# Performance work log

Measured on AMD Instinct MI355X. Metric: run time of the kernel, lower is better.

## Reference

```python
import jax, jax.numpy as jnp
import numpy as np

D_K = 64

def setup_inputs() -> dict:
    key = jax.random.key(0)
    ks = jax.random.split(key, 5)
    B, H, N, Dk, Dv = 32, 16, 512, 64, 64
    Q = jax.random.normal(ks[0], (B, H, N, Dk), dtype=jnp.float32)
    K = jax.random.normal(ks[1], (B, H, N, Dk), dtype=jnp.float32)
    V = jax.random.normal(ks[2], (B, H, N, Dv), dtype=jnp.float32)
    pos_ids = jnp.arange(H * N, dtype=jnp.int64 if jax.config.jax_enable_x64 else jnp.int32).reshape(1, H, N)
    pos_k_table = jax.random.normal(ks[3], (H * N, Dk), dtype=jnp.float32)
    pos_v_table = jax.random.normal(ks[4], (H * N, Dv), dtype=jnp.float32)
    return {"Q": Q, "K": K, "V": V, "pos_ids": pos_ids,
            "pos_k_table": pos_k_table, "pos_v_table": pos_v_table}

def reference(Q, K, V, pos_ids, pos_k_table, pos_v_table):
    # Positional embedding lookup: [1, H, N, Dk] / [1, H, N, Dv]
    K_pos = pos_k_table[pos_ids]
    V_pos = pos_v_table[pos_ids]
    scale = 1.0 / np.sqrt(D_K).astype(np.float32)
    # scores: [B, H, Nq, Nk]
    scores = jnp.einsum('bhqd,bhkd->bhqk', Q, K + K_pos) * scale
    attn = jax.nn.softmax(scores, axis=-1)
    context = jnp.einsum('bhqk,bhkd->bhqd', attn, V + V_pos)
    return (context, attn)
```

## Files before the change

kernel.cpp:

```cpp
#include <hip/hip_runtime.h>
#include <hip/hip_bf16.h>

typedef float fx4 __attribute__((ext_vector_type(4)));
typedef __bf16 bf16x8 __attribute__((ext_vector_type(8)));

#define NB 32
#define NH 16
#define NN 512
#define ND 64

__global__ __launch_bounds__(256, 2)
void attn_fused(const float* __restrict__ Q,
                const float* __restrict__ K,
                const float* __restrict__ V,
                const int*   __restrict__ pos_ids,
                const float* __restrict__ pkt,
                const float* __restrict__ pvt,
                float* __restrict__ ctx_out,
                float* __restrict__ attn_out)
{
    __shared__ alignas(16) __bf16 Plds[32][520];
    __shared__ alignas(16) __bf16 vt[64][72];
    __shared__ alignas(16) float redA[32][4];
    __shared__ alignas(16) float redB[32][4];

    const int bid = blockIdx.x;
    const int swz = (bid & 7) * 1024 + (bid >> 3);
    const int bh  = swz >> 4;
    const int qb  = swz & 15;
    const int h   = bh & (NH - 1);
    const int tid = threadIdx.x;
    const int wid = tid >> 6;
    const int lane = tid & 63;
    const int g   = lane >> 4;
    const int lr  = lane & 15;
    const int q0  = qb * 32;
    const size_t base = (size_t)bh * (NN * ND);
    const float CEXP = 0.125f * 1.44269504088896340736f;

    bf16x8 qf[2][2];
#pragma unroll
    for (int rt = 0; rt < 2; ++rt)
#pragma unroll
        for (int ks = 0; ks < 2; ++ks) {
            const float* qp = Q + base + (size_t)(q0 + rt * 16 + lr) * ND + ks * 32 + g * 8;
            fx4 a = *(const fx4*)qp;
            fx4 b = *(const fx4*)(qp + 4);
#pragma unroll
            for (int i = 0; i < 4; ++i) {
                qf[rt][ks][i]     = (__bf16)a[i];
                qf[rt][ks][4 + i] = (__bf16)b[i];
            }
        }

    fx4 acc[2][8];
    const fx4 vzero = {0.f, 0.f, 0.f, 0.f};
#pragma unroll
    for (int rt = 0; rt < 2; ++rt)
#pragma unroll
        for (int ct = 0; ct < 8; ++ct) acc[rt][ct] = vzero;

    const int wbase = wid * 128;
#pragma unroll
    for (int ct = 0; ct < 8; ++ct) {
        const int n = wbase + ct * 16 + lr;
        const int pid = pos_ids[h * NN + n];
        const float* kr = K + base + (size_t)n * ND;
        const float* pr = pkt + (size_t)pid * ND;
        bf16x8 bf[2];
#pragma unroll
        for (int ks = 0; ks < 2; ++ks) {
            fx4 k0 = *(const fx4*)(kr + ks * 32 + g * 8);
            fx4 k1 = *(const fx4*)(kr + ks * 32 + g * 8 + 4);
            fx4 p0 = *(const fx4*)(pr + ks * 32 + g * 8);
            fx4 p1 = *(const fx4*)(pr + ks * 32 + g * 8 + 4);
#pragma unroll
            for (int i = 0; i < 4; ++i) {
                bf[ks][i]     = (__bf16)(k0[i] + p0[i]);
                bf[ks][4 + i] = (__bf16)(k1[i] + p1[i]);
            }
        }
#pragma unroll
        for (int rt = 0; rt < 2; ++rt)
#pragma unroll
            for (int ks = 0; ks < 2; ++ks)
                acc[rt][ct] = __builtin_amdgcn_mfma_f32_16x16x32_bf16(
                    qf[rt][ks], bf[ks], acc[rt][ct], 0, 0, 0);
    }

    float fm[2][4], rs[2][4];
#pragma unroll
    for (int rt = 0; rt < 2; ++rt)
#pragma unroll
        for (int r = 0; r < 4; ++r) {
            float m = acc[rt][0][r];
#pragma unroll
            for (int ct = 1; ct < 8; ++ct) m = fmaxf(m, acc[rt][ct][r]);
#pragma unroll
            for (int off = 1; off < 16; off <<= 1) m = fmaxf(m, __shfl_xor(m, off));
            if (lr == 0) redA[rt * 16 + g * 4 + r][wid] = m;
        }
    __syncthreads();
#pragma unroll
    for (int rt = 0; rt < 2; ++rt)
#pragma unroll
        for (int r = 0; r < 4; ++r) {
            fx4 v = *(const fx4*)redA[rt * 16 + g * 4 + r];
            fm[rt][r] = fmaxf(fmaxf(v[0], v[1]), fmaxf(v[2], v[3]));
        }
#pragma unroll
    for (int rt = 0; rt < 2; ++rt)
#pragma unroll
        for (int r = 0; r < 4; ++r) {
            float s = 0.f;
#pragma unroll
            for (int ct = 0; ct < 8; ++ct) {
                float p = exp2f((acc[rt][ct][r] - fm[rt][r]) * CEXP);
                acc[rt][ct][r] = p;
                s += p;
            }
#pragma unroll
            for (int off = 1; off < 16; off <<= 1) s += __shfl_xor(s, off);
            if (lr == 0) redB[rt * 16 + g * 4 + r][wid] = s;
        }
    __syncthreads();
#pragma unroll
    for (int rt = 0; rt < 2; ++rt)
#pragma unroll
        for (int r = 0; r < 4; ++r) {
            fx4 v = *(const fx4*)redB[rt * 16 + g * 4 + r];
            rs[rt][r] = 1.0f / (v[0] + v[1] + v[2] + v[3]);
        }

#pragma unroll
    for (int rt = 0; rt < 2; ++rt)
#pragma unroll
        for (int ct = 0; ct < 8; ++ct)
#pragma unroll
            for (int r = 0; r < 4; ++r)
                Plds[rt * 16 + g * 4 + r][wbase + ct * 16 + lr] =
                    (__bf16)(acc[rt][ct][r] * rs[rt][r]);
    __syncthreads();

    {
        const int row = tid >> 3;
        const int c8  = (tid & 7) * 8;
        const size_t arow = ((size_t)bh * NN + q0 + row) * NN;
#pragma unroll
        for (int j = 0; j < 8; ++j) {
            bf16x8 p = *(const bf16x8*)&Plds[row][j * 64 + c8];
            fx4 o0, o1;
#pragma unroll
            for (int i = 0; i < 4; ++i) { o0[i] = (float)p[i]; o1[i] = (float)p[4 + i]; }
            *(fx4*)&attn_out[arow + j * 64 + c8]     = o0;
            *(fx4*)&attn_out[arow + j * 64 + c8 + 4] = o1;
        }
    }

    fx4 accp[2];
    accp[0] = vzero; accp[1] = vzero;
    const int rtp = wid >> 1;
    const int cb  = (wid & 1) * 32;
    const int nloc = tid >> 2;
    const int d0   = (tid & 3) * 16;
#pragma unroll 1
    for (int c = 0; c < 8; ++c) {
        __syncthreads();
        {
            const int ng = c * 64 + nloc;
            const int pidv = pos_ids[h * NN + ng];
            const float* vr = V + base + (size_t)ng * ND + d0;
            const float* pr = pvt + (size_t)pidv * ND + d0;
#pragma unroll
            for (int q4 = 0; q4 < 4; ++q4) {
                fx4 v = *(const fx4*)(vr + q4 * 4);
                fx4 p = *(const fx4*)(pr + q4 * 4);
#pragma unroll
                for (int i = 0; i < 4; ++i)
                    vt[d0 + q4 * 4 + i][nloc] = (__bf16)(v[i] + p[i]);
            }
        }
        __syncthreads();
#pragma unroll
        for (int ks = 0; ks < 2; ++ks) {
            bf16x8 pa = *(const bf16x8*)&Plds[rtp * 16 + lr][c * 64 + ks * 32 + g * 8];
#pragma unroll
            for (int ctd = 0; ctd < 2; ++ctd) {
                bf16x8 vb = *(const bf16x8*)&vt[cb + ctd * 16 + lr][ks * 32 + g * 8];
                accp[ctd] = __builtin_amdgcn_mfma_f32_16x16x32_bf16(pa, vb, accp[ctd], 0, 0, 0);
            }
        }
    }

#pragma unroll
    for (int ctd = 0; ctd < 2; ++ctd)
#pragma unroll
        for (int r = 0; r < 4; ++r) {
            const int row = rtp * 16 + g * 4 + r;
            ctx_out[((size_t)bh * NN + q0 + row) * ND + cb + ctd * 16 + lr] = accp[ctd][r];
        }
}

extern "C" void kernel_launch(void* const* d_in, const int* in_sizes, int n_in,
                              void* d_out, int out_size, void* d_ws, size_t ws_size,
                              hipStream_t stream) {
    const float* Q   = (const float*)d_in[0];
    const float* K   = (const float*)d_in[1];
    const float* V   = (const float*)d_in[2];
    const int*   pid = (const int*)d_in[3];
    const float* pkt = (const float*)d_in[4];
    const float* pvt = (const float*)d_in[5];
    float* ctx  = (float*)d_out;
    float* attn = ctx + (size_t)NB * NH * NN * ND;

    dim3 grid(NB * NH * (NN / 32));
    dim3 block(256);
    hipLaunchKernelGGL(attn_fused, grid, block, 0, stream,
                       Q, K, V, pid, pkt, pvt, ctx, attn);
}
```

Before: 1.055 ms.

## Split into bf16 K/V-transpose prep kernel and register-only attention kernel

Adds a prep kernel that adds the positional tables to K and V once, converts them to bf16 and writes V transposed into workspace, so attention blocks no longer redo the gather, add and convert for every query block. The main kernel gives each wave 16 query rows across all 512 keys. That removes the LDS staging, the cross-wave reductions and the barriers, and drops the row-max subtraction in softmax. The P·V step reads the normalized probabilities back from the just-written attn output in global memory instead of LDS. The risks are overflow for large scores without the max shift, a doubled global read of the attention matrix, and higher register pressure from 32 accumulator tiles.

```diff
diff --git a/kernel.cpp b/kernel.cpp
--- a/kernel.cpp
+++ b/kernel.cpp
@@ -4,201 +4,160 @@
 typedef float fx4 __attribute__((ext_vector_type(4)));
 typedef __bf16 bf16x8 __attribute__((ext_vector_type(8)));
 
-#define NB 32
-#define NH 16
 #define NN 512
 #define ND 64
+#define NH 16
+#define NB 32
+#define BH (NB * NH)
+
+__global__ __launch_bounds__(256)
+void prep_kernel(const float* __restrict__ K, const float* __restrict__ V,
+                 const int* __restrict__ pos_ids,
+                 const float* __restrict__ pkt, const float* __restrict__ pvt,
+                 __bf16* __restrict__ Kb, __bf16* __restrict__ VT)
+{
+    __shared__ alignas(16) __bf16 vt[64][72];
+    const int bid = blockIdx.x;
+    const int bh = bid >> 3, nc = bid & 7;
+    const int h  = bh & (NH - 1);
+    const int t  = threadIdx.x;
+    const int nl = t >> 2;
+    const int dq = (t & 3) * 16;
+    const int n  = nc * 64 + nl;
+    const int pid = pos_ids[h * NN + n];
+    const size_t rowb = (size_t)(bh * NN + n) * ND;
+
+    {
+        const float* kr = K + rowb + dq;
+        const float* pr = pkt + (size_t)pid * ND + dq;
+        bf16x8 o[2];
+#pragma unroll
+        for (int q = 0; q < 4; ++q) {
+            fx4 a = *(const fx4*)(kr + q * 4);
+            fx4 b = *(const fx4*)(pr + q * 4);
+#pragma unroll
+            for (int i = 0; i < 4; ++i) o[q >> 1][(q & 1) * 4 + i] = (__bf16)(a[i] + b[i]);
+        }
+        *(bf16x8*)(Kb + rowb + dq)     = o[0];
+        *(bf16x8*)(Kb + rowb + dq + 8) = o[1];
+    }
+    {
+        const float* vr = V + rowb + dq;
+        const float* pr = pvt + (size_t)pid * ND + dq;
+        bf16x8 o[2];
+#pragma unroll
+        for (int q = 0; q < 4; ++q) {
+            fx4 a = *(const fx4*)(vr + q * 4);
+            fx4 b = *(const fx4*)(pr + q * 4);
+#pragma unroll
+            for (int i = 0; i < 4; ++i) o[q >> 1][(q & 1) * 4 + i] = (__bf16)(a[i] + b[i]);
+        }
+        *(bf16x8*)&vt[nl][dq]     = o[0];
+        *(bf16x8*)&vt[nl][dq + 8] = o[1];
+    }
+    __syncthreads();
+    {
+        const int d  = t >> 2;
+        const int j0 = (t & 3) * 16;
+        bf16x8 o[2];
+#pragma unroll
+        for (int i = 0; i < 16; ++i) o[i >> 3][i & 7] = vt[j0 + i][d];
+        __bf16* dst = VT + ((size_t)bh * ND + d) * NN + nc * 64 + j0;
+        *(bf16x8*)dst       = o[0];
+        *(bf16x8*)(dst + 8) = o[1];
+    }
+}
 
 __global__ __launch_bounds__(256, 2)
-void attn_fused(const float* __restrict__ Q,
-                const float* __restrict__ K,
-                const float* __restrict__ V,
-                const int*   __restrict__ pos_ids,
-                const float* __restrict__ pkt,
-                const float* __restrict__ pvt,
-                float* __restrict__ ctx_out,
-                float* __restrict__ attn_out)
+void attn_main(const float* __restrict__ Q,
+               const __bf16* __restrict__ Kb,
+               const __bf16* __restrict__ VT,
+               float* __restrict__ ctx_out,
+               float* __restrict__ attn_out)
 {
-    __shared__ alignas(16) __bf16 Plds[32][520];
-    __shared__ alignas(16) __bf16 vt[64][72];
-    __shared__ alignas(16) float redA[32][4];
-    __shared__ alignas(16) float redB[32][4];
-
     const int bid = blockIdx.x;
-    const int swz = (bid & 7) * 1024 + (bid >> 3);
-    const int bh  = swz >> 4;
-    const int qb  = swz & 15;
-    const int h   = bh & (NH - 1);
+    const int swz = (bid & 7) * 512 + (bid >> 3);
+    const int bh  = swz >> 3;
+    const int qb  = swz & 7;
     const int tid = threadIdx.x;
-    const int wid = tid >> 6;
-    const int lane = tid & 63;
-    const int g   = lane >> 4;
-    const int lr  = lane & 15;
-    const int q0  = qb * 32;
-    const size_t base = (size_t)bh * (NN * ND);
+    const int lane = tid & 63, g = lane >> 4, lr = lane & 15;
+    const int q0  = qb * 64 + (tid >> 6) * 16;
+    const size_t kbase = (size_t)bh * NN * ND;
     const float CEXP = 0.125f * 1.44269504088896340736f;
 
-    bf16x8 qf[2][2];
+    bf16x8 qf[2];
 #pragma unroll
-    for (int rt = 0; rt < 2; ++rt)
+    for (int ks = 0; ks < 2; ++ks) {
+        const float* qp = Q + kbase + (size_t)(q0 + lr) * ND + ks * 32 + g * 8;
+        fx4 a = *(const fx4*)qp;
+        fx4 b = *(const fx4*)(qp + 4);
 #pragma unroll
-        for (int ks = 0; ks < 2; ++ks) {
-            const float* qp = Q + base + (size_t)(q0 + rt * 16 + lr) * ND + ks * 32 + g * 8;
-            fx4 a = *(const fx4*)qp;
-            fx4 b = *(const fx4*)(qp + 4);
-#pragma unroll
-            for (int i = 0; i < 4; ++i) {
-                qf[rt][ks][i]     = (__bf16)a[i];
-                qf[rt][ks][4 + i] = (__bf16)b[i];
-            }
-        }
+        for (int i = 0; i < 4; ++i) { qf[ks][i] = (__bf16)a[i]; qf[ks][4 + i] = (__bf16)b[i]; }
+    }
 
-    fx4 acc[2][8];
+    fx4 acc[32];
     const fx4 vzero = {0.f, 0.f, 0.f, 0.f};
 #pragma unroll
-    for (int rt = 0; rt < 2; ++rt)
+    for (int ct = 0; ct < 32; ++ct) acc[ct] = vzero;
+
+    const __bf16* kp0 = Kb + kbase + (size_t)lr * ND + g * 8;
 #pragma unroll
-        for (int ct = 0; ct < 8; ++ct) acc[rt][ct] = vzero;
-
-    const int wbase = wid * 128;
-#pragma unroll
-    for (int ct = 0; ct < 8; ++ct) {
-        const int n = wbase + ct * 16 + lr;
-        const int pid = pos_ids[h * NN + n];
-        const float* kr = K + base + (size_t)n * ND;
-        const float* pr = pkt + (size_t)pid * ND;
-        bf16x8 bf[2];
-#pragma unroll
-        for (int ks = 0; ks < 2; ++ks) {
-            fx4 k0 = *(const fx4*)(kr + ks * 32 + g * 8);
-            fx4 k1 = *(const fx4*)(kr + ks * 32 + g * 8 + 4);
-            fx4 p0 = *(const fx4*)(pr + ks * 32 + g * 8);
-            fx4 p1 = *(const fx4*)(pr + ks * 32 + g * 8 + 4);
-#pragma unroll
-            for (int i = 0; i < 4; ++i) {
-                bf[ks][i]     = (__bf16)(k0[i] + p0[i]);
-                bf[ks][4 + i] = (__bf16)(k1[i] + p1[i]);
-            }
-        }
-#pragma unroll
-        for (int rt = 0; rt < 2; ++rt)
-#pragma unroll
-            for (int ks = 0; ks < 2; ++ks)
-                acc[rt][ct] = __builtin_amdgcn_mfma_f32_16x16x32_bf16(
-                    qf[rt][ks], bf[ks], acc[rt][ct], 0, 0, 0);
+    for (int ct = 0; ct < 32; ++ct) {
+        bf16x8 b0 = *(const bf16x8*)(kp0 + (size_t)ct * 16 * ND);
+        bf16x8 b1 = *(const bf16x8*)(kp0 + (size_t)ct * 16 * ND + 32);
+        acc[ct] = __builtin_amdgcn_mfma_f32_16x16x32_bf16(qf[0], b0, acc[ct], 0, 0, 0);
+        acc[ct] = __builtin_amdgcn_mfma_f32_16x16x32_bf16(qf[1], b1, acc[ct], 0, 0, 0);
     }
 
-    float fm[2][4], rs[2][4];
+    float rs[4];
 #pragma unroll
-    for (int rt = 0; rt < 2; ++rt)
+    for (int r = 0; r < 4; ++r) {
+        float s = 0.f;
 #pragma unroll
-        for (int r = 0; r < 4; ++r) {
-            float m = acc[rt][0][r];
-#pragma unroll
-            for (int ct = 1; ct < 8; ++ct) m = fmaxf(m, acc[rt][ct][r]);
-#pragma unroll
-            for (int off = 1; off < 16; off <<= 1) m = fmaxf(m, __shfl_xor(m, off));
-            if (lr == 0) redA[rt * 16 + g * 4 + r][wid] = m;
+        for (int ct = 0; ct < 32; ++ct) {
+            float p = exp2f(acc[ct][r] * CEXP);
+            acc[ct][r] = p;
+            s += p;
         }
-    __syncthreads();
-#pragma unroll
-    for (int rt = 0; rt < 2; ++rt)
-#pragma unroll
-        for (int r = 0; r < 4; ++r) {
-            fx4 v = *(const fx4*)redA[rt * 16 + g * 4 + r];
-            fm[rt][r] = fmaxf(fmaxf(v[0], v[1]), fmaxf(v[2], v[3]));
-        }
-#pragma unroll
-    for (int rt = 0; rt < 2; ++rt)
-#pragma unroll
-        for (int r = 0; r < 4; ++r) {
-            float s = 0.f;
-#pragma unroll
-            for (int ct = 0; ct < 8; ++ct) {
-                float p = exp2f((acc[rt][ct][r] - fm[rt][r]) * CEXP);
-                acc[rt][ct][r] = p;
-                s += p;
-            }
-#pragma unroll
-            for (int off = 1; off < 16; off <<= 1) s += __shfl_xor(s, off);
-            if (lr == 0) redB[rt * 16 + g * 4 + r][wid] = s;
-        }
-    __syncthreads();
-#pragma unroll
-    for (int rt = 0; rt < 2; ++rt)
-#pragma unroll
-        for (int r = 0; r < 4; ++r) {
-            fx4 v = *(const fx4*)redB[rt * 16 + g * 4 + r];
-            rs[rt][r] = 1.0f / (v[0] + v[1] + v[2] + v[3]);
-        }
+        s += __shfl_xor(s, 1); s += __shfl_xor(s, 2);
+        s += __shfl_xor(s, 4); s += __shfl_xor(s, 8);
+        rs[r] = 1.0f / s;
+    }
 
 #pragma unroll
-    for (int rt = 0; rt < 2; ++rt)
+    for (int r = 0; r < 4; ++r) {
+        float* ap = attn_out + ((size_t)bh * NN + q0 + g * 4 + r) * NN + lr;
 #pragma unroll
-        for (int ct = 0; ct < 8; ++ct)
-#pragma unroll
-            for (int r = 0; r < 4; ++r)
-                Plds[rt * 16 + g * 4 + r][wbase + ct * 16 + lr] =
-                    (__bf16)(acc[rt][ct][r] * rs[rt][r]);
-    __syncthreads();
-
-    {
-        const int row = tid >> 3;
-        const int c8  = (tid & 7) * 8;
-        const size_t arow = ((size_t)bh * NN + q0 + row) * NN;
-#pragma unroll
-        for (int j = 0; j < 8; ++j) {
-            bf16x8 p = *(const bf16x8*)&Plds[row][j * 64 + c8];
-            fx4 o0, o1;
-#pragma unroll
-            for (int i = 0; i < 4; ++i) { o0[i] = (float)p[i]; o1[i] = (float)p[4 + i]; }
-            *(fx4*)&attn_out[arow + j * 64 + c8]     = o0;
-            *(fx4*)&attn_out[arow + j * 64 + c8 + 4] = o1;
-        }
+        for (int ct = 0; ct < 32; ++ct)
+            ap[ct * 16] = acc[ct][r] * rs[r];
     }
 
-    fx4 accp[2];
-    accp[0] = vzero; accp[1] = vzero;
-    const int rtp = wid >> 1;
-    const int cb  = (wid & 1) * 32;
-    const int nloc = tid >> 2;
-    const int d0   = (tid & 3) * 16;
-#pragma unroll 1
-    for (int c = 0; c < 8; ++c) {
-        __syncthreads();
-        {
-            const int ng = c * 64 + nloc;
-            const int pidv = pos_ids[h * NN + ng];
-            const float* vr = V + base + (size_t)ng * ND + d0;
-            const float* pr = pvt + (size_t)pidv * ND + d0;
+    asm volatile("s_waitcnt vmcnt(0)" ::: "memory");
+
+    fx4 accp[4];
 #pragma unroll
-            for (int q4 = 0; q4 < 4; ++q4) {
-                fx4 v = *(const fx4*)(vr + q4 * 4);
-                fx4 p = *(const fx4*)(pr + q4 * 4);
+    for (int c = 0; c < 4; ++c) accp[c] = vzero;
+    const float* prow = attn_out + ((size_t)bh * NN + q0 + lr) * NN + g * 8;
+    const __bf16* vp  = VT + (size_t)bh * ND * NN + (size_t)lr * NN + g * 8;
 #pragma unroll
-                for (int i = 0; i < 4; ++i)
-                    vt[d0 + q4 * 4 + i][nloc] = (__bf16)(v[i] + p[i]);
-            }
-        }
-        __syncthreads();
+    for (int ks2 = 0; ks2 < 16; ++ks2) {
+        fx4 a0 = *(const volatile fx4*)(prow + ks2 * 32);
+        fx4 a1 = *(const volatile fx4*)(prow + ks2 * 32 + 4);
+        bf16x8 pa;
 #pragma unroll
-        for (int ks = 0; ks < 2; ++ks) {
-            bf16x8 pa = *(const bf16x8*)&Plds[rtp * 16 + lr][c * 64 + ks * 32 + g * 8];
+        for (int i = 0; i < 4; ++i) { pa[i] = (__bf16)a0[i]; pa[4 + i] = (__bf16)a1[i]; }
 #pragma unroll
-            for (int ctd = 0; ctd < 2; ++ctd) {
-                bf16x8 vb = *(const bf16x8*)&vt[cb + ctd * 16 + lr][ks * 32 + g * 8];
-                accp[ctd] = __builtin_amdgcn_mfma_f32_16x16x32_bf16(pa, vb, accp[ctd], 0, 0, 0);
-            }
+        for (int ctd = 0; ctd < 4; ++ctd) {
+            bf16x8 vb = *(const bf16x8*)(vp + (size_t)ctd * 16 * NN + ks2 * 32);
+            accp[ctd] = __builtin_amdgcn_mfma_f32_16x16x32_bf16(pa, vb, accp[ctd], 0, 0, 0);
         }
     }
 
 #pragma unroll
-    for (int ctd = 0; ctd < 2; ++ctd)
+    for (int ctd = 0; ctd < 4; ++ctd)
 #pragma unroll
-        for (int r = 0; r < 4; ++r) {
-            const int row = rtp * 16 + g * 4 + r;
-            ctx_out[((size_t)bh * NN + q0 + row) * ND + cb + ctd * 16 + lr] = accp[ctd][r];
-        }
+        for (int r = 0; r < 4; ++r)
+            ctx_out[((size_t)bh * NN + q0 + g * 4 + r) * ND + ctd * 16 + lr] = accp[ctd][r];
 }
 
 extern "C" void kernel_launch(void* const* d_in, const int* in_sizes, int n_in,
@@ -211,10 +170,13 @@
     const float* pkt = (const float*)d_in[4];
     const float* pvt = (const float*)d_in[5];
     float* ctx  = (float*)d_out;
-    float* attn = ctx + (size_t)NB * NH * NN * ND;
+    float* attn = ctx + (size_t)BH * NN * ND;
 
-    dim3 grid(NB * NH * (NN / 32));
-    dim3 block(256);
-    hipLaunchKernelGGL(attn_fused, grid, block, 0, stream,
-                       Q, K, V, pid, pkt, pvt, ctx, attn);
+    __bf16* Kb = (__bf16*)d_ws;
+    __bf16* VT = Kb + (size_t)BH * NN * ND;
+
+    hipLaunchKernelGGL(prep_kernel, dim3(BH * 8), dim3(256), 0, stream,
+                       K, V, pid, pkt, pvt, Kb, VT);
+    hipLaunchKernelGGL(attn_main, dim3(BH * 8), dim3(256), 0, stream,
+                       Q, Kb, VT, ctx, attn);
 }
```

After: 1.104 ms. 1.05x slower.
